# Kernel optimization log

Measured on AMD Instinct MI355X. Metric: run time of the kernel, lower is better.

Reference implementation:

```python
import jax, jax.numpy as jnp
import numpy as np

NUM_HEADS = 12


def setup_inputs() -> dict:
    key = jax.random.key(0)
    ks = jax.random.split(key, 5)
    B, N, D = 8, 1024, 768
    x = jax.random.normal(ks[0], (B, N, D), dtype=jnp.float32)
    w_qkv = jax.random.normal(ks[1], (D, 3 * D), dtype=jnp.float32) * (D ** -0.5)
    b_qkv = jax.random.normal(ks[2], (3 * D,), dtype=jnp.float32) * 0.02
    w_proj = jax.random.normal(ks[3], (D, D), dtype=jnp.float32) * (D ** -0.5)
    b_proj = jax.random.normal(ks[4], (D,), dtype=jnp.float32) * 0.02
    return {"x": x, "w_qkv": w_qkv, "b_qkv": b_qkv, "w_proj": w_proj, "b_proj": b_proj}


def reference(x, w_qkv, b_qkv, w_proj, b_proj):
    B, N, D = x.shape
    H = NUM_HEADS
    hd = D // H
    scale = hd ** -0.5
    qkv = x @ w_qkv + b_qkv                      # [B, N, 3D]
    qkv = qkv.reshape(B, N, 3, H, hd)
    q, k, v = jnp.moveaxis(qkv, 2, 0)            # each [B, N, H, hd]
    # scores: [B, H, N, N]
    scores = jnp.einsum("bqhd,bkhd->bhqk", q, k) * scale
    attn = jax.nn.softmax(scores, axis=-1)
    a = jnp.einsum("bhqk,bkhd->bqhd", attn, v)   # [B, N, H, hd]
    a = a.reshape(B, N, D)
    return a @ w_proj + b_proj
```

## Files before the change

kernel.cpp:

```cpp
#include <hip/hip_runtime.h>

#define B_ 8
#define N_ 1024
#define D_ 768
#define H_ 12
#define HD 64
#define M_ (B_*N_)

typedef short short8 __attribute__((ext_vector_type(8)));
typedef float f32x4 __attribute__((ext_vector_type(4)));
typedef float f32x16 __attribute__((ext_vector_type(16)));
typedef int int4v __attribute__((ext_vector_type(4)));

__device__ __forceinline__ unsigned short f2bf(float f) {
    union { float f; unsigned int u; } c; c.f = f;
    unsigned int u = c.u;
    unsigned int r = (u + 0x7fffu + ((u >> 16) & 1u)) >> 16;
    return (unsigned short)r;
}

__device__ __forceinline__ float exp2_hw(float x) {
    float r;
    asm("v_exp_f32 %0, %1" : "=v"(r) : "v"(x));
    return r;
}

__device__ __forceinline__ unsigned int cvtpk_bf16(float a, float b) {
    unsigned int r;
    asm("v_cvt_pk_bf16_f32 %0, %1, %2" : "=v"(r) : "v"(a), "v"(b));
    return r;
}

#define PLSWAP(a, b) asm volatile("v_permlane32_swap_b32 %0, %1" : "+&v"(a), "+&v"(b))

__device__ __forceinline__ short8 pack4(unsigned int a, unsigned int b,
                                        unsigned int c, unsigned int d) {
    union { int4v i; short8 s; } u;
    u.i = (int4v){(int)a, (int)b, (int)c, (int)d};
    return u.s;
}

__device__ __forceinline__ void gload16(const void* g, void* l) {
    __builtin_amdgcn_global_load_lds(
        (const __attribute__((address_space(1))) unsigned int*)g,
        (__attribute__((address_space(3))) unsigned int*)l, 16, 0, 0);
}


__global__ __launch_bounds__(256) void prep_kernel(
    const float* __restrict__ x, const float* __restrict__ wqkv,
    const float* __restrict__ wproj,
    unsigned short* __restrict__ xb, unsigned short* __restrict__ wqkvT,
    unsigned short* __restrict__ wprojT)
{
    int bid = blockIdx.x, tid = threadIdx.x;
    if (bid < 6144) {
        int i = bid * 256 + tid;
        float4 v = reinterpret_cast<const float4*>(x)[i];
        ushort4 o;
        o.x = f2bf(v.x); o.y = f2bf(v.y); o.z = f2bf(v.z); o.w = f2bf(v.w);
        reinterpret_cast<ushort4*>(xb)[i] = o;
    } else if (bid < 6144 + 6912) {
        int i = (bid - 6144) * 256 + tid;
        int r = i / 2304, c = i - r * 2304;
        wqkvT[c * 768 + r] = f2bf(wqkv[i]);
    } else {
        int i = (bid - 13056) * 256 + tid;
        int r = i / 768, c = i - r * 768;
        wprojT[c * 768 + r] = f2bf(wproj[i]);
    }
}


template<int MODE>
__global__ __launch_bounds__(256) void gemm_kernel(
    const unsigned short* __restrict__ A,
    const unsigned short* __restrict__ Bt,
    const float* __restrict__ bias,
    float* __restrict__ outf,
    unsigned short* __restrict__ qo,
    unsigned short* __restrict__ ko,
    unsigned short* __restrict__ vo,
    int Ndim, int K)
{
    __shared__ alignas(16) unsigned short As[2][4096];
    __shared__ alignas(16) unsigned short Bs[2][4096];

    int tid = threadIdx.x;
    int lane = tid & 63, w = tid >> 6;
    int wr = w >> 1, wc = w & 1;

    int m0 = blockIdx.y * 128, n0 = blockIdx.x * 128;

    int lr = lane & 15, lk8 = (lane >> 4) * 8;
    int org = (lane >> 4) * 4;

    int srow = tid >> 2;
    int selem = (tid & 3) * 8;
    const unsigned short* gA = A + (size_t)(m0 + srow) * K + selem;
    const unsigned short* gB = Bt + (size_t)(n0 + srow) * K + selem;

    f32x4 acc[4][4] = {};

#define GSTAGE(buf, k0)                                                    \
    do {                                                                   \
        gload16(gA + (k0), &As[buf][w * 512]);                             \
        gload16(gA + (size_t)64 * K + (k0), &As[buf][2048 + w * 512]);     \
        gload16(gB + (k0), &Bs[buf][w * 512]);                             \
        gload16(gB + (size_t)64 * K + (k0), &Bs[buf][2048 + w * 512]);     \
    } while (0)

    GSTAGE(0, 0);
    asm volatile("s_waitcnt vmcnt(0)" ::: "memory");
    __builtin_amdgcn_s_barrier();
    __builtin_amdgcn_sched_barrier(0);

    int KT = K >> 5;
    int cur = 0;
    for (int kt = 0; kt < KT; ++kt) {
        if (kt + 1 < KT) GSTAGE(cur ^ 1, (kt + 1) * 32);

        short8 af[4], bf[4];
        #pragma unroll
        for (int mi = 0; mi < 4; mi++)
            af[mi] = *reinterpret_cast<const short8*>(&As[cur][(wr * 64 + mi * 16 + lr) * 32 + lk8]);
        #pragma unroll
        for (int ni = 0; ni < 4; ni++)
            bf[ni] = *reinterpret_cast<const short8*>(&Bs[cur][(wc * 64 + ni * 16 + lr) * 32 + lk8]);
        #pragma unroll
        for (int mi = 0; mi < 4; mi++)
            #pragma unroll
            for (int ni = 0; ni < 4; ni++)
                acc[mi][ni] = (MODE == 1)
                    ? __builtin_amdgcn_mfma_f32_16x16x32_bf16(bf[ni], af[mi], acc[mi][ni], 0, 0, 0)
                    : __builtin_amdgcn_mfma_f32_16x16x32_bf16(af[mi], bf[ni], acc[mi][ni], 0, 0, 0);

        if (kt + 1 < KT) {
            asm volatile("s_waitcnt vmcnt(0)" ::: "memory");
            __builtin_amdgcn_s_barrier();
            __builtin_amdgcn_sched_barrier(0);
            cur ^= 1;
        }
    }
#undef GSTAGE

    if (MODE == 1) {
        int m = m0 + wr * 64 + lr;
        #pragma unroll
        for (int mi = 0; mi < 4; mi++) {
            int row = m + mi * 16;
            #pragma unroll
            for (int ni = 0; ni < 4; ni++) {
                int col = n0 + wc * 64 + ni * 16 + org;
                float4 bv = *reinterpret_cast<const float4*>(&bias[col]);
                float4 o;
                o.x = acc[mi][ni][0] + bv.x;
                o.y = acc[mi][ni][1] + bv.y;
                o.z = acc[mi][ni][2] + bv.z;
                o.w = acc[mi][ni][3] + bv.w;
                *reinterpret_cast<float4*>(&outf[(size_t)row * Ndim + col]) = o;
            }
        }
        return;
    }

    if (n0 >= 1536) {
        #pragma unroll
        for (int mi = 0; mi < 4; mi++) {
            int nn0g = m0 + wr * 64 + mi * 16 + org;
            int b = nn0g >> 10, nn = nn0g & 1023;
            #pragma unroll
            for (int ni = 0; ni < 4; ni++) {
                int colg = n0 + wc * 64 + ni * 16 + lr;
                int rem = colg - 1536;
                int h = rem >> 6, dd = rem & 63;
                float bv = bias[colg];
                unsigned long long u = 0;
                #pragma unroll
                for (int r = 0; r < 4; r++)
                    u |= (unsigned long long)f2bf(acc[mi][ni][r] + bv) << (16 * r);
                *reinterpret_cast<unsigned long long*>(
                    vo + ((size_t)(b * H_ + h) * HD + dd) * N_ + nn) = u;
            }
        }
    } else {
        int which = n0 / 768;
        unsigned short* dst = (which == 0) ? qo : ko;
        float fold = (which == 0) ? 0.125f * 1.44269504088896f : 1.0f;
        #pragma unroll
        for (int mi = 0; mi < 4; mi++) {
            #pragma unroll
            for (int ni = 0; ni < 4; ni++) {
                int col = n0 + wc * 64 + ni * 16 + lr;
                int rem = col - which * 768;
                int h = rem >> 6, dd = rem & 63;
                float bv = bias[col];
                #pragma unroll
                for (int r = 0; r < 4; r++) {
                    int row = m0 + wr * 64 + mi * 16 + org + r;
                    int b = row >> 10, nn = row & 1023;
                    dst[(((size_t)(b * H_ + h) * N_ + nn) * HD) + dd] =
                        f2bf((acc[mi][ni][r] + bv) * fold);
                }
            }
        }
    }
}


__global__ __launch_bounds__(256) void attn_kernel(
    const unsigned short* __restrict__ qg,
    const unsigned short* __restrict__ kg,
    const unsigned short* __restrict__ vtg,
    unsigned short* __restrict__ aout)
{
    __shared__ alignas(16) unsigned short Ks[2][4096];
    __shared__ alignas(16) unsigned short Vs[2][4096];

    int tid = threadIdx.x;
    int lane = tid & 63, w = tid >> 6;

    int bid = blockIdx.x;
    int xcd = bid & 7;
    int chunk = bid >> 3;
    int bh = xcd * 12 + (chunk % 12);
    int qblk = chunk / 12;
    int b = bh / H_, h = bh - b * H_;
    int q0w = qblk * 128 + w * 32;
    int l31 = lane & 31;
    int hi = lane >> 5;
    int swz = l31 & 7;

    const unsigned short* qp = qg + ((size_t)bh * N_ + q0w + l31) * HD + hi * 8;
    short8 qf[4];
    #pragma unroll
    for (int ds = 0; ds < 4; ds++)
        qf[ds] = *reinterpret_cast<const short8*>(qp + ds * 16);

    const unsigned short* kbh = kg + (size_t)bh * N_ * HD;
    const unsigned short* vtbh = vtg + (size_t)bh * HD * N_;

    int sr0 = tid >> 3;
    int sj0 = (tid & 7) ^ (sr0 & 7);
    int sr1 = sr0 + 32;
    int sj1 = (tid & 7) ^ (sr1 & 7);

    float m_run = -INFINITY, l_run = 0.f;
    f32x16 o0 = {}, o1 = {};

#define STAGE(buf, kv0)                                                        \
    do {                                                                       \
        gload16(kbh + (size_t)((kv0) + sr0) * HD + sj0 * 8, &Ks[buf][w * 512]);\
        gload16(kbh + (size_t)((kv0) + sr1) * HD + sj1 * 8, &Ks[buf][2048 + w * 512]);\
        gload16(vtbh + (size_t)sr0 * N_ + (kv0) + sj0 * 8, &Vs[buf][w * 512]); \
        gload16(vtbh + (size_t)sr1 * N_ + (kv0) + sj1 * 8, &Vs[buf][2048 + w * 512]);\
    } while (0)

    STAGE(0, 0);
    asm volatile("s_waitcnt vmcnt(0)" ::: "memory");
    __builtin_amdgcn_s_barrier();
    __builtin_amdgcn_sched_barrier(0);

    int cur = 0;
    for (int t = 0; t < 16; ++t) {
        if (t < 15) STAGE(cur ^ 1, (t + 1) * 64);

        const unsigned short* Ksb = Ks[cur];
        const unsigned short* Vsb = Vs[cur];

        f32x16 s0 = {}, s1 = {};
        #pragma unroll
        for (int ds = 0; ds < 4; ds++) {
            int pc = (ds * 2 + hi) ^ swz;
            short8 kf0 = *reinterpret_cast<const short8*>(&Ksb[(l31) * 64 + pc * 8]);
            short8 kf1 = *reinterpret_cast<const short8*>(&Ksb[(32 + l31) * 64 + pc * 8]);
            s0 = __builtin_amdgcn_mfma_f32_32x32x16_bf16(kf0, qf[ds], s0, 0, 0, 0);
            s1 = __builtin_amdgcn_mfma_f32_32x32x16_bf16(kf1, qf[ds], s1, 0, 0, 0);
        }

        float mx = s0[0];
        #pragma unroll
        for (int r = 1; r < 16; r++) mx = fmaxf(mx, s0[r]);
        #pragma unroll
        for (int r = 0; r < 16; r++) mx = fmaxf(mx, s1[r]);
        mx = fmaxf(mx, __shfl_xor(mx, 32, 64));

        if (__any(mx > m_run + 8.f)) {
            float mn = fmaxf(m_run, mx);
            float al = exp2_hw(m_run - mn);
            m_run = mn;
            l_run *= al;
            o0 *= al;
            o1 *= al;
        }

        float psum = 0.f;
        #pragma unroll
        for (int r = 0; r < 16; r++) { float p = exp2_hw(s0[r] - m_run); psum += p; s0[r] = p; }
        #pragma unroll
        for (int r = 0; r < 16; r++) { float p = exp2_hw(s1[r] - m_run); psum += p; s1[r] = p; }

        l_run += psum + __shfl_xor(psum, 32, 64);

        unsigned int c0[8], c1[8];
        #pragma unroll
        for (int i = 0; i < 8; i++) c0[i] = cvtpk_bf16(s0[2 * i], s0[2 * i + 1]);
        #pragma unroll
        for (int i = 0; i < 8; i++) c1[i] = cvtpk_bf16(s1[2 * i], s1[2 * i + 1]);
        PLSWAP(c0[0], c0[2]); PLSWAP(c0[1], c0[3]);
        PLSWAP(c0[4], c0[6]); PLSWAP(c0[5], c0[7]);
        PLSWAP(c1[0], c1[2]); PLSWAP(c1[1], c1[3]);
        PLSWAP(c1[4], c1[6]); PLSWAP(c1[5], c1[7]);
        short8 pa0 = pack4(c0[0], c0[1], c0[2], c0[3]);
        short8 pa1 = pack4(c0[4], c0[5], c0[6], c0[7]);
        short8 pa2 = pack4(c1[0], c1[1], c1[2], c1[3]);
        short8 pa3 = pack4(c1[4], c1[5], c1[6], c1[7]);

        #pragma unroll
        for (int ks = 0; ks < 4; ks++) {
            int pc = (ks * 2 + hi) ^ swz;
            short8 vf0 = *reinterpret_cast<const short8*>(&Vsb[(l31) * 64 + pc * 8]);
            short8 vf1 = *reinterpret_cast<const short8*>(&Vsb[(32 + l31) * 64 + pc * 8]);
            short8 pa = (ks == 0) ? pa0 : (ks == 1) ? pa1 : (ks == 2) ? pa2 : pa3;
            o0 = __builtin_amdgcn_mfma_f32_32x32x16_bf16(vf0, pa, o0, 0, 0, 0);
            o1 = __builtin_amdgcn_mfma_f32_32x32x16_bf16(vf1, pa, o1, 0, 0, 0);
        }

        if (t < 15) {
            asm volatile("s_waitcnt vmcnt(0)" ::: "memory");
            __builtin_amdgcn_s_barrier();
            __builtin_amdgcn_sched_barrier(0);
            cur ^= 1;
        }
    }
#undef STAGE

    float linv = 1.0f / l_run;
    unsigned short* op = aout + ((size_t)(b * N_ + q0w + l31)) * D_ + h * HD;
    #pragma unroll
    for (int rg = 0; rg < 4; rg++) {
        int dbase = 8 * rg + 4 * hi;
        unsigned long long u0 = 0, u1 = 0;
        #pragma unroll
        for (int k = 0; k < 4; k++) {
            u0 |= (unsigned long long)f2bf(o0[rg * 4 + k] * linv) << (16 * k);
            u1 |= (unsigned long long)f2bf(o1[rg * 4 + k] * linv) << (16 * k);
        }
        *reinterpret_cast<unsigned long long*>(op + dbase) = u0;
        *reinterpret_cast<unsigned long long*>(op + 32 + dbase) = u1;
    }
}


extern "C" void kernel_launch(void* const* d_in, const int* in_sizes, int n_in,
                              void* d_out, int out_size, void* d_ws, size_t ws_size,
                              hipStream_t stream) {
    const float* x      = (const float*)d_in[0];
    const float* w_qkv  = (const float*)d_in[1];
    const float* b_qkv  = (const float*)d_in[2];
    const float* w_proj = (const float*)d_in[3];
    const float* b_proj = (const float*)d_in[4];
    float* out = (float*)d_out;

    char* ws = (char*)d_ws;
    unsigned short* xb     = (unsigned short*)(ws + 0);
    unsigned short* wqkvT  = (unsigned short*)(ws + 12582912);
    unsigned short* wprojT = (unsigned short*)(ws + 16121856);
    unsigned short* qb     = (unsigned short*)(ws + 17301504);
    unsigned short* kb     = (unsigned short*)(ws + 29884416);
    unsigned short* vtb    = (unsigned short*)(ws + 42467328);
    unsigned short* aout   = xb;

    prep_kernel<<<15360, 256, 0, stream>>>(x, w_qkv, w_proj, xb, wqkvT, wprojT);

    gemm_kernel<0><<<dim3(18, 64), 256, 0, stream>>>(
        xb, wqkvT, b_qkv, nullptr, qb, kb, vtb, 3 * D_, D_);

    attn_kernel<<<768, 256, 0, stream>>>(qb, kb, vtb, aout);

    gemm_kernel<1><<<dim3(6, 64), 256, 0, stream>>>(
        aout, wprojT, b_proj, out, nullptr, nullptr, nullptr, D_, D_);
}
```

Measured before the change: 146.8 us.

## Triple-buffer GEMM LDS staging and remap blocks across XCDs

Moves the GEMM K-loop from double to triple buffering, keeping two stages of global-to-LDS loads in flight and waiting with vmcnt(4) instead of draining every load. Launches a 1D grid and remaps block IDs so consecutive tiles land on the same XCD (block index modulo 8), aiming for better L2 reuse of the A and B tiles. This uses 50% more shared memory per block, which may lower occupancy.

```diff
diff --git a/kernel.cpp b/kernel.cpp
--- a/kernel.cpp
+++ b/kernel.cpp
@@ -83,14 +83,19 @@
     unsigned short* __restrict__ vo,
     int Ndim, int K)
 {
-    __shared__ alignas(16) unsigned short As[2][4096];
-    __shared__ alignas(16) unsigned short Bs[2][4096];
+    __shared__ alignas(16) unsigned short As[3 * 4096];
+    __shared__ alignas(16) unsigned short Bs[3 * 4096];
 
     int tid = threadIdx.x;
     int lane = tid & 63, w = tid >> 6;
     int wr = w >> 1, wc = w & 1;
 
-    int m0 = blockIdx.y * 128, n0 = blockIdx.x * 128;
+    int nbx = Ndim >> 7;
+    int nwg = gridDim.x;
+    int cpx = nwg >> 3;
+    int sbid = (blockIdx.x & 7) * cpx + (blockIdx.x >> 3);
+    int bx = sbid % nbx, by = sbid / nbx;
+    int m0 = by * 128, n0 = bx * 128;
 
     int lr = lane & 15, lk8 = (lane >> 4) * 8;
     int org = (lane >> 4) * 4;
@@ -104,29 +109,33 @@
 
 #define GSTAGE(buf, k0)                                                    \
     do {                                                                   \
-        gload16(gA + (k0), &As[buf][w * 512]);                             \
-        gload16(gA + (size_t)64 * K + (k0), &As[buf][2048 + w * 512]);     \
-        gload16(gB + (k0), &Bs[buf][w * 512]);                             \
-        gload16(gB + (size_t)64 * K + (k0), &Bs[buf][2048 + w * 512]);     \
+        gload16(gA + (k0), As + (buf) * 4096 + w * 512);                   \
+        gload16(gA + (size_t)64 * K + (k0), As + (buf) * 4096 + 2048 + w * 512);\
+        gload16(gB + (k0), Bs + (buf) * 4096 + w * 512);                   \
+        gload16(gB + (size_t)64 * K + (k0), Bs + (buf) * 4096 + 2048 + w * 512);\
     } while (0)
 
     GSTAGE(0, 0);
-    asm volatile("s_waitcnt vmcnt(0)" ::: "memory");
+    GSTAGE(1, 32);
+    asm volatile("s_waitcnt vmcnt(4)" ::: "memory");
     __builtin_amdgcn_s_barrier();
     __builtin_amdgcn_sched_barrier(0);
 
     int KT = K >> 5;
     int cur = 0;
     for (int kt = 0; kt < KT; ++kt) {
-        if (kt + 1 < KT) GSTAGE(cur ^ 1, (kt + 1) * 32);
-
+        int sb = cur + 2; if (sb >= 3) sb -= 3;
+        if (kt + 2 < KT) GSTAGE(sb, (kt + 2) * 32);
+
+        const unsigned short* Ab = As + cur * 4096;
+        const unsigned short* Bb = Bs + cur * 4096;
         short8 af[4], bf[4];
         #pragma unroll
         for (int mi = 0; mi < 4; mi++)
-            af[mi] = *reinterpret_cast<const short8*>(&As[cur][(wr * 64 + mi * 16 + lr) * 32 + lk8]);
+            af[mi] = *reinterpret_cast<const short8*>(&Ab[(wr * 64 + mi * 16 + lr) * 32 + lk8]);
         #pragma unroll
         for (int ni = 0; ni < 4; ni++)
-            bf[ni] = *reinterpret_cast<const short8*>(&Bs[cur][(wc * 64 + ni * 16 + lr) * 32 + lk8]);
+            bf[ni] = *reinterpret_cast<const short8*>(&Bb[(wc * 64 + ni * 16 + lr) * 32 + lk8]);
         #pragma unroll
         for (int mi = 0; mi < 4; mi++)
             #pragma unroll
@@ -136,10 +145,13 @@
                     : __builtin_amdgcn_mfma_f32_16x16x32_bf16(af[mi], bf[ni], acc[mi][ni], 0, 0, 0);
 
         if (kt + 1 < KT) {
-            asm volatile("s_waitcnt vmcnt(0)" ::: "memory");
+            if (kt + 2 < KT)
+                asm volatile("s_waitcnt vmcnt(4)" ::: "memory");
+            else
+                asm volatile("s_waitcnt vmcnt(0)" ::: "memory");
             __builtin_amdgcn_s_barrier();
             __builtin_amdgcn_sched_barrier(0);
-            cur ^= 1;
+            cur = (cur == 2) ? 0 : cur + 1;
         }
     }
 #undef GSTAGE
@@ -373,11 +385,11 @@
 
     prep_kernel<<<15360, 256, 0, stream>>>(x, w_qkv, w_proj, xb, wqkvT, wprojT);
 
-    gemm_kernel<0><<<dim3(18, 64), 256, 0, stream>>>(
+    gemm_kernel<0><<<1152, 256, 0, stream>>>(
         xb, wqkvT, b_qkv, nullptr, qb, kb, vtb, 3 * D_, D_);
 
     attn_kernel<<<768, 256, 0, stream>>>(qb, kb, vtb, aout);
 
-    gemm_kernel<1><<<dim3(6, 64), 256, 0, stream>>>(
+    gemm_kernel<1><<<384, 256, 0, stream>>>(
         aout, wprojT, b_proj, out, nullptr, nullptr, nullptr, D_, D_);
 }
```

After: 145.8 us. About the same (-0.7%).
